# Performance work log

Measured on AMD Instinct MI355X. Metric: run time of the kernel, lower is better.

The kernel has to match this reference:

```python
import jax, jax.numpy as jnp
import numpy as np

K = 9  # 3x3 kernel taps

def conv2d(x, w, b):
    # stride 1, padding 1, NCHW / OIHW
    out = jax.lax.conv_general_dilated(x, w, (1, 1), ((1, 1), (1, 1)),
                                       dimension_numbers=('NCHW', 'OIHW', 'NCHW'))
    return out + b[None, :, None, None]

def deform_conv2d(x, offset, mask, w, b):
    # torchvision modulated deformable conv, kernel 3x3, stride 1, pad 1, dilation 1
    B, C, H, W = x.shape
    off = offset.reshape(B, K, 2, H, W)  # per-tap (dy, dx)
    ii = (jnp.arange(K) // 3).astype(x.dtype) - 1.0  # kernel row offset (pad=1)
    jj = (jnp.arange(K) % 3).astype(x.dtype) - 1.0   # kernel col offset
    hh = jnp.arange(H, dtype=x.dtype)[None, None, :, None]
    ww = jnp.arange(W, dtype=x.dtype)[None, None, None, :]
    py = hh + ii[None, :, None, None] + off[:, :, 0]  # [B,K,H,W] sample rows
    px = ww + jj[None, :, None, None] + off[:, :, 1]  # [B,K,H,W] sample cols

    y0 = jnp.floor(py); x0 = jnp.floor(px)
    dy = py - y0; dx = px - x0
    y0 = y0.astype(jnp.int32); x0 = x0.astype(jnp.int32)

    xf = x.reshape(B, C, H * W)

    def gather(yi, xi):
        valid = ((yi >= 0) & (yi < H) & (xi >= 0) & (xi < W)).astype(x.dtype)
        yc = jnp.clip(yi, 0, H - 1)
        xc = jnp.clip(xi, 0, W - 1)
        idx = (yc * W + xc).reshape(B, K * H * W)
        v = jax.vmap(lambda xb, ib: xb[:, ib])(xf, idx)  # [B,C,K*H*W]
        return v.reshape(B, C, K, H, W) * valid[:, None]

    v00 = gather(y0,     x0)
    v01 = gather(y0,     x0 + 1)
    v10 = gather(y0 + 1, x0)
    v11 = gather(y0 + 1, x0 + 1)

    dy = dy[:, None]; dx = dx[:, None]  # broadcast over channel dim
    val = (v00 * (1 - dy) * (1 - dx) + v01 * (1 - dy) * dx
           + v10 * dy * (1 - dx) + v11 * dy * dx)
    val = val * mask[:, None]  # sigmoid modulation, [B,1,K,H,W]

    out = jnp.einsum('ock,bckhw->bohw', w.reshape(w.shape[0], C, K), val)
    return out + b[None, :, None, None]

def setup_inputs() -> dict:
    key = jax.random.key(0)
    k1, k2, k3 = jax.random.split(key, 3)
    x = jax.random.normal(k1, (8, 3, 512, 512), dtype=jnp.float32)
    w_off = jax.random.normal(k2, (27, 3, 3, 3), dtype=jnp.float32) * 0.05
    b_off = jnp.zeros((27,), dtype=jnp.float32)
    w_def = jax.random.normal(k3, (3, 3, 3, 3), dtype=jnp.float32) * 0.1
    b_def = jnp.zeros((3,), dtype=jnp.float32)
    return {'x': x, 'w_off': w_off, 'b_off': b_off, 'w_def': w_def, 'b_def': b_def}

def reference(x, w_off, b_off, w_def, b_def):
    ow = conv2d(x, w_off, b_off)            # [B,27,H,W]
    offset = ow[:, :18]                      # 2*9 offsets
    mask = jax.nn.sigmoid(ow[:, 18:])        # 9 modulation masks
    return deform_conv2d(x, offset, mask, w_def, b_def)
```

## Files before the change

### kernel.cpp

```cpp
#include <hip/hip_runtime.h>
#include <math.h>

typedef float f2 __attribute__((ext_vector_type(2)));
typedef float f2u __attribute__((ext_vector_type(2), aligned(4)));
typedef float f4 __attribute__((ext_vector_type(4)));

#define BN 8
#define CIN 3
#define HH 512
#define WW 512
#define KK 9
#define OFFC 27
#define PATCH 27
#define TAPBLK 84

__global__ void reorder_weights(const float* __restrict__ w_off, float* __restrict__ ws)
{
    for (int idx = threadIdx.x; idx < KK * TAPBLK; idx += blockDim.x) {
        const int k = idx / TAPBLK;
        const int r = idx % TAPBLK;
        float v = 0.0f;
        if (r < 56) {
            const int q = r >> 1, half = r & 1;
            if (q < PATCH) v = w_off[(2 * k + half) * PATCH + q];
        } else {
            const int i = r - 56;
            if (i < PATCH) v = w_off[(18 + k) * PATCH + i];
        }
        ws[idx] = v;
    }
}

__global__ __launch_bounds__(256) void deform_fused_kernel(
    const float* __restrict__ x,
    const float* __restrict__ wsw,
    const float* __restrict__ b_off,
    const float* __restrict__ w_def,
    const float* __restrict__ b_def,
    float* __restrict__ out)
{
    __shared__ __attribute__((aligned(16))) float s_w[KK * TAPBLK];
    __shared__ f2 s_boyx[KK];
    __shared__ float s_bom[KK];
    __shared__ f2 s_wd01[PATCH];
    __shared__ float s_wd2[PATCH];
    __shared__ float s_bdef[3];

    {
        const int tid = threadIdx.x;
        const f4* src4 = (const f4*)wsw;
        f4* dst4 = (f4*)s_w;
        for (int i = tid; i < KK * TAPBLK / 4; i += blockDim.x) dst4[i] = src4[i];
        if (tid < KK) {
            f2 bp = { b_off[2 * tid], b_off[2 * tid + 1] };
            s_boyx[tid] = bp;
            s_bom[tid] = b_off[18 + tid];
        }
        if (tid < PATCH) {
            f2 wd = { w_def[tid], w_def[PATCH + tid] };
            s_wd01[tid] = wd;
            s_wd2[tid] = w_def[2 * PATCH + tid];
        }
        if (tid < 3) s_bdef[tid] = b_def[tid];
    }
    __syncthreads();

    const int w = blockIdx.x * blockDim.x + threadIdx.x;
    const int h = blockIdx.y;
    const int b = blockIdx.z;

    const size_t plane = (size_t)HH * WW;
    const float* xb = x + (size_t)b * CIN * plane;

    float patch[28];
    patch[27] = 0.0f;
    #pragma unroll
    for (int c = 0; c < CIN; ++c) {
        const float* xp = xb + c * plane;
        #pragma unroll
        for (int t = 0; t < KK; ++t) {
            const int yy = h + t / 3 - 1;
            const int xx = w + t % 3 - 1;
            const bool in = (yy >= 0) & (yy < HH) & (xx >= 0) & (xx < WW);
            patch[c * KK + t] = in ? xp[yy * WW + xx] : 0.0f;
        }
    }

    f2 acc01 = { s_bdef[0], s_bdef[1] };
    float acc2 = s_bdef[2];

    #pragma unroll 1
    for (int k = 0; k < KK; ++k) {
        f2 oyx = s_boyx[k];
        float om = s_bom[k];

        const f4* pw = (const f4*)&s_w[k * TAPBLK];
        #pragma unroll
        for (int j = 0; j < 14; ++j) {
            const f4 wq = pw[j];
            const float p0 = patch[2 * j];
            const float p1 = patch[2 * j + 1];
            const f2 w0 = { wq.x, wq.y };
            const f2 w1 = { wq.z, wq.w };
            const f2 pp0 = { p0, p0 };
            const f2 pp1 = { p1, p1 };
            oyx = __builtin_elementwise_fma(w0, pp0, oyx);
            oyx = __builtin_elementwise_fma(w1, pp1, oyx);
        }
        const f4* pm = (const f4*)&s_w[k * TAPBLK + 56];
        #pragma unroll
        for (int j = 0; j < 7; ++j) {
            const f4 wm4 = pm[j];
            om = fmaf(wm4.x, patch[4 * j],     om);
            om = fmaf(wm4.y, patch[4 * j + 1], om);
            om = fmaf(wm4.z, patch[4 * j + 2], om);
            om = fmaf(wm4.w, patch[4 * j + 3], om);
        }

        const float m = 1.0f / (1.0f + __expf(-om));

        const float py = (float)h + (float)(k / 3 - 1) + oyx.x;
        const float px = (float)w + (float)(k % 3 - 1) + oyx.y;
        const float y0f = floorf(py);
        const float x0f = floorf(px);
        const float dy = py - y0f;
        const float dx = px - x0f;
        const int y0 = (int)y0f;
        const int x0 = (int)x0f;

        const f2 dxp = { 1.0f - dx, dx };
        const f2 wT = dxp * (1.0f - dy);
        const f2 wB = dxp * dy;

        const int interior = (y0 >= 0) & (y0 + 1 < HH) & (x0 >= 0) & (x0 + 1 < WW);

        if (__all(interior)) {
            const int idx = y0 * WW + x0;
            #pragma unroll
            for (int c = 0; c < CIN; ++c) {
                const float* xp = xb + c * plane + idx;
                const f2 vT = *(const f2u*)(xp);
                const f2 vB = *(const f2u*)(xp + WW);
                f2 s = vT * wT;
                s = __builtin_elementwise_fma(vB, wB, s);
                const float val = (s.x + s.y) * m;
                const f2 vv = { val, val };
                acc01 = __builtin_elementwise_fma(s_wd01[c * KK + k], vv, acc01);
                acc2 = fmaf(s_wd2[c * KK + k], val, acc2);
            }
        } else {
            const bool vy0 = (y0 >= 0)     & (y0 < HH);
            const bool vy1 = (y0 + 1 >= 0) & (y0 + 1 < HH);
            const bool vx0 = (x0 >= 0)     & (x0 < WW);
            const bool vx1 = (x0 + 1 >= 0) & (x0 + 1 < WW);

            const int yc0 = min(max(y0, 0), HH - 1);
            const int yc1 = min(max(y0 + 1, 0), HH - 1);
            const int xc0 = min(max(x0, 0), WW - 1);
            const int xc1 = min(max(x0 + 1, 0), WW - 1);

            #pragma unroll
            for (int c = 0; c < CIN; ++c) {
                const float* xp = xb + c * plane;
                const float v00 = (vy0 & vx0) ? xp[yc0 * WW + xc0] : 0.0f;
                const float v01 = (vy0 & vx1) ? xp[yc0 * WW + xc1] : 0.0f;
                const float v10 = (vy1 & vx0) ? xp[yc1 * WW + xc0] : 0.0f;
                const float v11 = (vy1 & vx1) ? xp[yc1 * WW + xc1] : 0.0f;

                const float val =
                    (v00 * wT.x + v01 * wT.y + v10 * wB.x + v11 * wB.y) * m;
                const f2 vv = { val, val };
                acc01 = __builtin_elementwise_fma(s_wd01[c * KK + k], vv, acc01);
                acc2 = fmaf(s_wd2[c * KK + k], val, acc2);
            }
        }
    }

    const size_t base = (size_t)b * (CIN * plane) + (size_t)h * WW + w;
    out[base]             = acc01.x;
    out[base + plane]     = acc01.y;
    out[base + 2 * plane] = acc2;
}

extern "C" void kernel_launch(void* const* d_in, const int* in_sizes, int n_in,
                              void* d_out, int out_size, void* d_ws, size_t ws_size,
                              hipStream_t stream) {
    const float* x     = (const float*)d_in[0];
    const float* w_off = (const float*)d_in[1];
    const float* b_off = (const float*)d_in[2];
    const float* w_def = (const float*)d_in[3];
    const float* b_def = (const float*)d_in[4];
    float* out = (float*)d_out;
    float* wsw = (float*)d_ws;

    reorder_weights<<<1, 256, 0, stream>>>(w_off, wsw);

    dim3 block(256, 1, 1);
    dim3 grid(WW / 256, HH, BN);
    deform_fused_kernel<<<grid, block, 0, stream>>>(x, wsw, b_off, w_def, b_def, out);
}
```

Baseline: 187.8 us.

## Compute two output rows per thread and pack all weights into shared block

Each thread now handles two vertically adjacent output pixels. It loads a 4-row by 3-column neighbourhood per channel once and shares it between the two offset/mask convolutions, so each weight read from LDS feeds two pixels. Deformable-conv weights and offset biases are also packed into the per-tap shared block, so they come in through one vectorised load. This halves the grid and cuts redundant patch loads and LDS traffic, at the cost of more registers per thread and lower occupancy.

```diff
diff --git a/kernel.cpp b/kernel.cpp
--- a/kernel.cpp
+++ b/kernel.cpp
@@ -10,11 +10,13 @@
 #define HH 512
 #define WW 512
 #define KK 9
-#define OFFC 27
 #define PATCH 27
-#define TAPBLK 84
-
-__global__ void reorder_weights(const float* __restrict__ w_off, float* __restrict__ ws)
+#define TAPBLK 100
+
+__global__ void reorder_weights(const float* __restrict__ w_off,
+                                const float* __restrict__ b_off,
+                                const float* __restrict__ w_def,
+                                float* __restrict__ ws)
 {
     for (int idx = threadIdx.x; idx < KK * TAPBLK; idx += blockDim.x) {
         const int k = idx / TAPBLK;
@@ -23,163 +25,196 @@
         if (r < 56) {
             const int q = r >> 1, half = r & 1;
             if (q < PATCH) v = w_off[(2 * k + half) * PATCH + q];
-        } else {
+        } else if (r < 84) {
             const int i = r - 56;
             if (i < PATCH) v = w_off[(18 + k) * PATCH + i];
+        } else if (r < 96) {
+            const int j = r - 84;
+            const int c = j >> 2, o = j & 3;
+            if (o < 3) v = w_def[o * PATCH + c * KK + k];
+        } else {
+            const int e = r - 96;
+            if (e == 0)      v = b_off[2 * k];
+            else if (e == 1) v = b_off[2 * k + 1];
+            else if (e == 2) v = b_off[18 + k];
         }
         ws[idx] = v;
+    }
+}
+
+#define PA(i) ((i) < PATCH ? rows[((i) / 9) * 12 + (((i) % 9) / 3) * 3 + ((i) % 3)] : 0.0f)
+#define PB(i) ((i) < PATCH ? rows[((i) / 9) * 12 + (((i) % 9) / 3 + 1) * 3 + ((i) % 3)] : 0.0f)
+
+__device__ __forceinline__ void tap_px(
+    const float* __restrict__ xb, const size_t plane,
+    const int hpx, const int w, const int k,
+    const f2 oyx, const float om,
+    const f4* wd,
+    f2& acc01, float& acc2)
+{
+    const float m = 1.0f / (1.0f + __expf(-om));
+
+    const float py = (float)hpx + (float)(k / 3 - 1) + oyx.x;
+    const float px = (float)w   + (float)(k % 3 - 1) + oyx.y;
+    const float y0f = floorf(py);
+    const float x0f = floorf(px);
+    const float dy = py - y0f;
+    const float dx = px - x0f;
+    const int y0 = (int)y0f;
+    const int x0 = (int)x0f;
+
+    const f2 dxp = { 1.0f - dx, dx };
+    const f2 wT = dxp * (1.0f - dy);
+    const f2 wB = dxp * dy;
+
+    const int interior = (y0 >= 0) & (y0 + 1 < HH) & (x0 >= 0) & (x0 + 1 < WW);
+
+    if (__all(interior)) {
+        const int idx = y0 * WW + x0;
+        #pragma unroll
+        for (int c = 0; c < CIN; ++c) {
+            const float* xp = xb + c * plane + idx;
+            const f2 vT = *(const f2u*)(xp);
+            const f2 vB = *(const f2u*)(xp + WW);
+            f2 s = vT * wT;
+            s = __builtin_elementwise_fma(vB, wB, s);
+            const float val = (s.x + s.y) * m;
+            const f4 wq = wd[c];
+            const f2 w01 = { wq.x, wq.y };
+            const f2 vv = { val, val };
+            acc01 = __builtin_elementwise_fma(w01, vv, acc01);
+            acc2 = fmaf(wq.z, val, acc2);
+        }
+    } else {
+        const bool vy0 = (y0 >= 0)     & (y0 < HH);
+        const bool vy1 = (y0 + 1 >= 0) & (y0 + 1 < HH);
+        const bool vx0 = (x0 >= 0)     & (x0 < WW);
+        const bool vx1 = (x0 + 1 >= 0) & (x0 + 1 < WW);
+
+        const int yc0 = min(max(y0, 0), HH - 1);
+        const int yc1 = min(max(y0 + 1, 0), HH - 1);
+        const int xc0 = min(max(x0, 0), WW - 1);
+        const int xc1 = min(max(x0 + 1, 0), WW - 1);
+
+        #pragma unroll
+        for (int c = 0; c < CIN; ++c) {
+            const float* xp = xb + c * plane;
+            const float v00 = (vy0 & vx0) ? xp[yc0 * WW + xc0] : 0.0f;
+            const float v01 = (vy0 & vx1) ? xp[yc0 * WW + xc1] : 0.0f;
+            const float v10 = (vy1 & vx0) ? xp[yc1 * WW + xc0] : 0.0f;
+            const float v11 = (vy1 & vx1) ? xp[yc1 * WW + xc1] : 0.0f;
+
+            const float val =
+                (v00 * wT.x + v01 * wT.y + v10 * wB.x + v11 * wB.y) * m;
+            const f4 wq = wd[c];
+            const f2 w01 = { wq.x, wq.y };
+            const f2 vv = { val, val };
+            acc01 = __builtin_elementwise_fma(w01, vv, acc01);
+            acc2 = fmaf(wq.z, val, acc2);
+        }
     }
 }
 
 __global__ __launch_bounds__(256) void deform_fused_kernel(
     const float* __restrict__ x,
     const float* __restrict__ wsw,
-    const float* __restrict__ b_off,
-    const float* __restrict__ w_def,
     const float* __restrict__ b_def,
     float* __restrict__ out)
 {
     __shared__ __attribute__((aligned(16))) float s_w[KK * TAPBLK];
-    __shared__ f2 s_boyx[KK];
-    __shared__ float s_bom[KK];
-    __shared__ f2 s_wd01[PATCH];
-    __shared__ float s_wd2[PATCH];
     __shared__ float s_bdef[3];
 
     {
         const int tid = threadIdx.x;
         const f4* src4 = (const f4*)wsw;
         f4* dst4 = (f4*)s_w;
-        for (int i = tid; i < KK * TAPBLK / 4; i += blockDim.x) dst4[i] = src4[i];
-        if (tid < KK) {
-            f2 bp = { b_off[2 * tid], b_off[2 * tid + 1] };
-            s_boyx[tid] = bp;
-            s_bom[tid] = b_off[18 + tid];
-        }
-        if (tid < PATCH) {
-            f2 wd = { w_def[tid], w_def[PATCH + tid] };
-            s_wd01[tid] = wd;
-            s_wd2[tid] = w_def[2 * PATCH + tid];
-        }
+        if (tid < KK * TAPBLK / 4) dst4[tid] = src4[tid];
         if (tid < 3) s_bdef[tid] = b_def[tid];
     }
     __syncthreads();
 
     const int w = blockIdx.x * blockDim.x + threadIdx.x;
-    const int h = blockIdx.y;
+    const int h0 = 2 * blockIdx.y;
     const int b = blockIdx.z;
 
     const size_t plane = (size_t)HH * WW;
     const float* xb = x + (size_t)b * CIN * plane;
 
-    float patch[28];
-    patch[27] = 0.0f;
+    float rows[CIN * 12];
     #pragma unroll
     for (int c = 0; c < CIN; ++c) {
         const float* xp = xb + c * plane;
         #pragma unroll
-        for (int t = 0; t < KK; ++t) {
-            const int yy = h + t / 3 - 1;
-            const int xx = w + t % 3 - 1;
-            const bool in = (yy >= 0) & (yy < HH) & (xx >= 0) & (xx < WW);
-            patch[c * KK + t] = in ? xp[yy * WW + xx] : 0.0f;
-        }
-    }
-
-    f2 acc01 = { s_bdef[0], s_bdef[1] };
-    float acc2 = s_bdef[2];
+        for (int d = 0; d < 4; ++d) {
+            const int yy = h0 - 1 + d;
+            #pragma unroll
+            for (int e = 0; e < 3; ++e) {
+                const int xx = w - 1 + e;
+                const bool in = (yy >= 0) & (yy < HH) & (xx >= 0) & (xx < WW);
+                rows[c * 12 + d * 3 + e] = in ? xp[yy * WW + xx] : 0.0f;
+            }
+        }
+    }
+
+    f2 accA01 = { s_bdef[0], s_bdef[1] };
+    float accA2 = s_bdef[2];
+    f2 accB01 = accA01;
+    float accB2 = accA2;
 
     #pragma unroll 1
     for (int k = 0; k < KK; ++k) {
-        f2 oyx = s_boyx[k];
-        float om = s_bom[k];
-
-        const f4* pw = (const f4*)&s_w[k * TAPBLK];
+        const float* blk = &s_w[k * TAPBLK];
+        const f4* pw = (const f4*)blk;
+        const f4* pm = (const f4*)(blk + 56);
+        const f4* wd = (const f4*)(blk + 84);
+        const f4 bias = *(const f4*)(blk + 96);
+
+        f2 oyxA = { bias.x, bias.y };
+        f2 oyxB = oyxA;
+        float omA = bias.z, omB = bias.z;
+
         #pragma unroll
         for (int j = 0; j < 14; ++j) {
             const f4 wq = pw[j];
-            const float p0 = patch[2 * j];
-            const float p1 = patch[2 * j + 1];
             const f2 w0 = { wq.x, wq.y };
             const f2 w1 = { wq.z, wq.w };
-            const f2 pp0 = { p0, p0 };
-            const f2 pp1 = { p1, p1 };
-            oyx = __builtin_elementwise_fma(w0, pp0, oyx);
-            oyx = __builtin_elementwise_fma(w1, pp1, oyx);
-        }
-        const f4* pm = (const f4*)&s_w[k * TAPBLK + 56];
+            {
+                const float a0 = PA(2 * j), a1 = PA(2 * j + 1);
+                const f2 p0 = { a0, a0 }, p1 = { a1, a1 };
+                oyxA = __builtin_elementwise_fma(w0, p0, oyxA);
+                oyxA = __builtin_elementwise_fma(w1, p1, oyxA);
+            }
+            {
+                const float b0 = PB(2 * j), b1 = PB(2 * j + 1);
+                const f2 p0 = { b0, b0 }, p1 = { b1, b1 };
+                oyxB = __builtin_elementwise_fma(w0, p0, oyxB);
+                oyxB = __builtin_elementwise_fma(w1, p1, oyxB);
+            }
+        }
         #pragma unroll
         for (int j = 0; j < 7; ++j) {
             const f4 wm4 = pm[j];
-            om = fmaf(wm4.x, patch[4 * j],     om);
-            om = fmaf(wm4.y, patch[4 * j + 1], om);
-            om = fmaf(wm4.z, patch[4 * j + 2], om);
-            om = fmaf(wm4.w, patch[4 * j + 3], om);
-        }
-
-        const float m = 1.0f / (1.0f + __expf(-om));
-
-        const float py = (float)h + (float)(k / 3 - 1) + oyx.x;
-        const float px = (float)w + (float)(k % 3 - 1) + oyx.y;
-        const float y0f = floorf(py);
-        const float x0f = floorf(px);
-        const float dy = py - y0f;
-        const float dx = px - x0f;
-        const int y0 = (int)y0f;
-        const int x0 = (int)x0f;
-
-        const f2 dxp = { 1.0f - dx, dx };
-        const f2 wT = dxp * (1.0f - dy);
-        const f2 wB = dxp * dy;
-
-        const int interior = (y0 >= 0) & (y0 + 1 < HH) & (x0 >= 0) & (x0 + 1 < WW);
-
-        if (__all(interior)) {
-            const int idx = y0 * WW + x0;
-            #pragma unroll
-            for (int c = 0; c < CIN; ++c) {
-                const float* xp = xb + c * plane + idx;
-                const f2 vT = *(const f2u*)(xp);
-                const f2 vB = *(const f2u*)(xp + WW);
-                f2 s = vT * wT;
-                s = __builtin_elementwise_fma(vB, wB, s);
-                const float val = (s.x + s.y) * m;
-                const f2 vv = { val, val };
-                acc01 = __builtin_elementwise_fma(s_wd01[c * KK + k], vv, acc01);
-                acc2 = fmaf(s_wd2[c * KK + k], val, acc2);
-            }
-        } else {
-            const bool vy0 = (y0 >= 0)     & (y0 < HH);
-            const bool vy1 = (y0 + 1 >= 0) & (y0 + 1 < HH);
-            const bool vx0 = (x0 >= 0)     & (x0 < WW);
-            const bool vx1 = (x0 + 1 >= 0) & (x0 + 1 < WW);
-
-            const int yc0 = min(max(y0, 0), HH - 1);
-            const int yc1 = min(max(y0 + 1, 0), HH - 1);
-            const int xc0 = min(max(x0, 0), WW - 1);
-            const int xc1 = min(max(x0 + 1, 0), WW - 1);
-
-            #pragma unroll
-            for (int c = 0; c < CIN; ++c) {
-                const float* xp = xb + c * plane;
-                const float v00 = (vy0 & vx0) ? xp[yc0 * WW + xc0] : 0.0f;
-                const float v01 = (vy0 & vx1) ? xp[yc0 * WW + xc1] : 0.0f;
-                const float v10 = (vy1 & vx0) ? xp[yc1 * WW + xc0] : 0.0f;
-                const float v11 = (vy1 & vx1) ? xp[yc1 * WW + xc1] : 0.0f;
-
-                const float val =
-                    (v00 * wT.x + v01 * wT.y + v10 * wB.x + v11 * wB.y) * m;
-                const f2 vv = { val, val };
-                acc01 = __builtin_elementwise_fma(s_wd01[c * KK + k], vv, acc01);
-                acc2 = fmaf(s_wd2[c * KK + k], val, acc2);
-            }
-        }
-    }
-
-    const size_t base = (size_t)b * (CIN * plane) + (size_t)h * WW + w;
-    out[base]             = acc01.x;
-    out[base + plane]     = acc01.y;
-    out[base + 2 * plane] = acc2;
+            omA = fmaf(wm4.x, PA(4 * j),     omA);
+            omA = fmaf(wm4.y, PA(4 * j + 1), omA);
+            omA = fmaf(wm4.z, PA(4 * j + 2), omA);
+            omA = fmaf(wm4.w, PA(4 * j + 3), omA);
+            omB = fmaf(wm4.x, PB(4 * j),     omB);
+            omB = fmaf(wm4.y, PB(4 * j + 1), omB);
+            omB = fmaf(wm4.z, PB(4 * j + 2), omB);
+            omB = fmaf(wm4.w, PB(4 * j + 3), omB);
+        }
+
+        tap_px(xb, plane, h0,     w, k, oyxA, omA, wd, accA01, accA2);
+        tap_px(xb, plane, h0 + 1, w, k, oyxB, omB, wd, accB01, accB2);
+    }
+
+    const size_t base = (size_t)b * (CIN * plane) + (size_t)h0 * WW + w;
+    out[base]                  = accA01.x;
+    out[base + plane]          = accA01.y;
+    out[base + 2 * plane]      = accA2;
+    out[base + WW]             = accB01.x;
+    out[base + WW + plane]     = accB01.y;
+    out[base + WW + 2 * plane] = accB2;
 }
 
 extern "C" void kernel_launch(void* const* d_in, const int* in_sizes, int n_in,
@@ -193,9 +228,9 @@
     float* out = (float*)d_out;
     float* wsw = (float*)d_ws;
 
-    reorder_weights<<<1, 256, 0, stream>>>(w_off, wsw);
+    reorder_weights<<<1, 256, 0, stream>>>(w_off, b_off, w_def, wsw);
 
     dim3 block(256, 1, 1);
-    dim3 grid(WW / 256, HH, BN);
-    deform_fused_kernel<<<grid, block, 0, stream>>>(x, wsw, b_off, w_def, b_def, out);
-}
+    dim3 grid(WW / 256, HH / 2, BN);
+    deform_fused_kernel<<<grid, block, 0, stream>>>(x, wsw, b_def, out);
+}
```

Result: slower. 209.3 us (+11.4%).
